# Performance work log

Hardware: AMD Instinct MI355X
Metric: run time of the kernel (lower is better)

## Reference

```python
import jax, jax.numpy as jnp
import numpy as np

B, NQ, NK, D = 4, 4096, 4096, 256


def setup_inputs() -> dict:
    key = jax.random.key(0)
    ks = jax.random.split(key, 14)
    s = 1.0 / np.sqrt(D)
    def lin(k):
        kw, kb = jax.random.split(k)
        return (jax.random.uniform(kw, (D, D), jnp.float32, -s, s),
                jax.random.uniform(kb, (D,), jnp.float32, -s, s))
    Wq, bq = lin(ks[0]); Wk, bk = lin(ks[1]); Wv, bv = lin(ks[2])
    W1, b1 = lin(ks[3]); W2, b2 = lin(ks[4]); W3, b3 = lin(ks[5])
    x = jax.random.normal(ks[6], (B, NK, D), jnp.float32)
    query = jax.random.normal(ks[7], (B, NQ, D), jnp.float32)
    return {"x": x, "query": query,
            "Wq": Wq, "bq": bq, "Wk": Wk, "bk": bk, "Wv": Wv, "bv": bv,
            "W1": W1, "b1": b1, "W2": W2, "b2": b2, "W3": W3, "b3": b3}


def reference(x, query, Wq, bq, Wk, bk, Wv, bv, W1, b1, W2, b2, W3, b3):
    # Linear: y = x @ W.T + b (torch convention)
    q = jnp.einsum('bnd,ed->bne', query, Wq) + bq   # [B,NQ,D]
    k = jnp.einsum('bnd,ed->bne', x, Wk) + bk       # [B,NK,D]
    v = jnp.einsum('bnd,ed->bne', x, Wv) + bv       # [B,NK,D]
    scale = 1.0 / jnp.sqrt(jnp.float32(x.shape[-1]))
    scores = jnp.einsum('bqd,bkd->bqk', q, k) * scale  # [B,NQ,NK]
    attn = jax.nn.softmax(scores, axis=-1)
    out = jnp.einsum('bqk,bkd->bqd', attn, v)          # [B,NQ,D]
    h = jax.nn.relu(jnp.einsum('bqd,ed->bqe', out, W1) + b1)
    h = jax.nn.relu(jnp.einsum('bqd,ed->bqe', h, W2) + b2)
    h = jax.nn.relu(jnp.einsum('bqd,ed->bqe', h, W3) + b3)
    return h, attn
```

## Files before the change

### kernel.cpp

```cpp
#include <hip/hip_runtime.h>

typedef _Float16 h16;
typedef __attribute__((ext_vector_type(4))) _Float16 h16x4;
typedef __attribute__((ext_vector_type(8))) _Float16 h16x8;
typedef __attribute__((ext_vector_type(4))) float f32x4;

#define NQD 4194304L
#define NROWS 16384L
#define NKK 4096L

static __device__ __forceinline__ f32x4 mfma16(h16x8 a, h16x8 b, f32x4 c) {
  return __builtin_amdgcn_mfma_f32_16x16x32_f16(a, b, c, 0, 0, 0);
}

__global__ void cast_weights(const float* __restrict__ w0, const float* __restrict__ w1,
                             const float* __restrict__ w2, const float* __restrict__ w3,
                             const float* __restrict__ w4, const float* __restrict__ w5,
                             h16* __restrict__ dst) {
  int wi = blockIdx.y;
  const float* src = wi == 0 ? w0 : wi == 1 ? w1 : wi == 2 ? w2 : wi == 3 ? w3 : wi == 4 ? w4 : w5;
  int c = blockIdx.x * 256 + threadIdx.x;
  float4 v = ((const float4*)src)[c];
  h16x4 h = {(h16)v.x, (h16)v.y, (h16)v.z, (h16)v.w};
  *(h16x4*)&dst[(long)wi * 65536 + (long)c * 4] = h;
}

__global__ __launch_bounds__(256) void qkv_proj(const float* __restrict__ x,
                                                const float* __restrict__ qry,
                                                const h16* __restrict__ wh,
                                                const float* __restrict__ bq,
                                                const float* __restrict__ bk,
                                                const float* __restrict__ bv,
                                                h16* __restrict__ qh,
                                                h16* __restrict__ kh,
                                                h16* __restrict__ vT) {
  const int z = blockIdx.z;
  const float* A = (z == 0) ? qry : x;
  const h16* W = wh + (long)z * 65536;
  const float* bias = (z == 0) ? bq : (z == 1) ? bk : bv;
  h16* outH = (z == 0) ? qh : (z == 1) ? kh : nullptr;
  h16* outT = (z == 2) ? vT : nullptr;

  __shared__ h16 smem[128 * 72 + 64 * 72];
  h16 (*As)[72] = (h16(*)[72])smem;
  h16 (*Bs)[72] = (h16(*)[72])(smem + 128 * 72);
  const int tid = threadIdx.x;
  const int wave = tid >> 6, lane = tid & 63;
  const int quad = lane >> 4, l16 = lane & 15;
  const long arow0 = (long)blockIdx.x * 128;
  const int bn = blockIdx.y;
  f32x4 acc[2][4] = {};
  for (int k0 = 0; k0 < 256; k0 += 64) {
    #pragma unroll
    for (int it = 0; it < 8; ++it) {
      int c = it * 256 + tid;
      int r = c >> 4, c4 = (c & 15) * 4;
      float4 v = *(const float4*)&A[(arow0 + r) * 256 + k0 + c4];
      h16x4 h = {(h16)v.x, (h16)v.y, (h16)v.z, (h16)v.w};
      *(h16x4*)&As[r][c4] = h;
    }
    #pragma unroll
    for (int it = 0; it < 2; ++it) {
      int c = it * 256 + tid;
      int r = c >> 3, c8 = (c & 7) * 8;
      *(h16x8*)&Bs[r][c8] = *(const h16x8*)&W[(long)(bn * 64 + r) * 256 + k0 + c8];
    }
    __syncthreads();
    #pragma unroll
    for (int ks = 0; ks < 64; ks += 32) {
      h16x8 a[2], b[4];
      #pragma unroll
      for (int mi = 0; mi < 2; ++mi)
        a[mi] = *(const h16x8*)&As[wave * 32 + mi * 16 + l16][ks + quad * 8];
      #pragma unroll
      for (int ni = 0; ni < 4; ++ni)
        b[ni] = *(const h16x8*)&Bs[ni * 16 + l16][ks + quad * 8];
      #pragma unroll
      for (int mi = 0; mi < 2; ++mi)
        #pragma unroll
        for (int ni = 0; ni < 4; ++ni)
          acc[mi][ni] = mfma16(a[mi], b[ni], acc[mi][ni]);
    }
    __syncthreads();
  }
  if (outH) {
    #pragma unroll
    for (int mi = 0; mi < 2; ++mi) {
      #pragma unroll
      for (int ni = 0; ni < 4; ++ni) {
        int n = bn * 64 + ni * 16 + l16;
        float bv_ = bias[n];
        #pragma unroll
        for (int i = 0; i < 4; ++i) {
          long m = arow0 + wave * 32 + mi * 16 + quad * 4 + i;
          outH[m * 256 + n] = (h16)(acc[mi][ni][i] + bv_);
        }
      }
    }
  } else {
    h16* stg = smem;
    #pragma unroll
    for (int mi = 0; mi < 2; ++mi) {
      #pragma unroll
      for (int ni = 0; ni < 4; ++ni) {
        int dl = ni * 16 + l16;
        float bv_ = bias[bn * 64 + dl];
        int mlb = wave * 32 + mi * 16 + quad * 4;
        h16x4 hv = {(h16)(acc[mi][ni][0] + bv_), (h16)(acc[mi][ni][1] + bv_),
                    (h16)(acc[mi][ni][2] + bv_), (h16)(acc[mi][ni][3] + bv_)};
        *(h16x4*)&stg[dl * 136 + mlb] = hv;
      }
    }
    __syncthreads();
    const int bb = (int)(arow0 >> 12);
    const long kb = arow0 & 4095;
    #pragma unroll
    for (int p = 0; p < 4; ++p) {
      int d = p * 16 + (tid >> 4);
      int c = (tid & 15) * 8;
      h16x8 v = *(const h16x8*)&stg[d * 136 + c];
      *(h16x8*)&outT[((long)bb * 256 + bn * 64 + d) * 4096 + kb + c] = v;
    }
  }
}

__global__ __launch_bounds__(256) void gemm256(const h16* __restrict__ A,
                                               const h16* __restrict__ W,
                                               const float* __restrict__ bias,
                                               h16* __restrict__ outH,
                                               float* __restrict__ outF) {
  __shared__ h16 As[128][72];
  __shared__ h16 Bs[64][72];
  const int tid = threadIdx.x;
  const int wave = tid >> 6, lane = tid & 63;
  const int quad = lane >> 4, l16 = lane & 15;
  const long arow0 = (long)blockIdx.x * 128;
  const int bn = blockIdx.y;
  f32x4 acc[2][4] = {};
  for (int k0 = 0; k0 < 256; k0 += 64) {
    #pragma unroll
    for (int it = 0; it < 4; ++it) {
      int c = it * 256 + tid;
      int r = c >> 3, c8 = (c & 7) * 8;
      *(h16x8*)&As[r][c8] = *(const h16x8*)&A[(arow0 + r) * 256 + k0 + c8];
    }
    #pragma unroll
    for (int it = 0; it < 2; ++it) {
      int c = it * 256 + tid;
      int r = c >> 3, c8 = (c & 7) * 8;
      *(h16x8*)&Bs[r][c8] = *(const h16x8*)&W[(long)(bn * 64 + r) * 256 + k0 + c8];
    }
    __syncthreads();
    #pragma unroll
    for (int ks = 0; ks < 64; ks += 32) {
      h16x8 a[2], b[4];
      #pragma unroll
      for (int mi = 0; mi < 2; ++mi)
        a[mi] = *(const h16x8*)&As[wave * 32 + mi * 16 + l16][ks + quad * 8];
      #pragma unroll
      for (int ni = 0; ni < 4; ++ni)
        b[ni] = *(const h16x8*)&Bs[ni * 16 + l16][ks + quad * 8];
      #pragma unroll
      for (int mi = 0; mi < 2; ++mi)
        #pragma unroll
        for (int ni = 0; ni < 4; ++ni)
          acc[mi][ni] = mfma16(a[mi], b[ni], acc[mi][ni]);
    }
    __syncthreads();
  }
  #pragma unroll
  for (int mi = 0; mi < 2; ++mi) {
    #pragma unroll
    for (int ni = 0; ni < 4; ++ni) {
      int n = bn * 64 + ni * 16 + l16;
      float bv = bias[n];
      #pragma unroll
      for (int i = 0; i < 4; ++i) {
        long m = arow0 + wave * 32 + mi * 16 + quad * 4 + i;
        float v = fmaxf(acc[mi][ni][i] + bv, 0.0f);
        if (outH) outH[m * 256 + n] = (h16)v;
        if (outF) outF[m * 256 + n] = v;
      }
    }
  }
}

__global__ __launch_bounds__(256) void gemm_scores(const h16* __restrict__ qh,
                                                   const h16* __restrict__ kh,
                                                   float2* __restrict__ stats,
                                                   h16* __restrict__ Sh,
                                                   float* __restrict__ Sf) {
  __shared__ h16 smem[128 * 72 * 2];
  h16 (*As)[72] = (h16(*)[72])smem;
  h16 (*Bs)[72] = (h16(*)[72])(smem + 128 * 72);
  const int tid = threadIdx.x;
  const int wave = tid >> 6, lane = tid & 63;
  const int quad = lane >> 4, l16 = lane & 15;
  const int bm = blockIdx.x, bn = blockIdx.y, b = blockIdx.z;
  const h16* Aq = qh + (long)b * 4096 * 256 + (long)bm * 128 * 256;
  const h16* Bk = kh + (long)b * 4096 * 256 + (long)bn * 128 * 256;
  f32x4 acc[2][8] = {};
  for (int k0 = 0; k0 < 256; k0 += 64) {
    #pragma unroll
    for (int it = 0; it < 4; ++it) {
      int c = it * 256 + tid;
      int r = c >> 3, c8 = (c & 7) * 8;
      *(h16x8*)&As[r][c8] = *(const h16x8*)&Aq[(long)r * 256 + k0 + c8];
      *(h16x8*)&Bs[r][c8] = *(const h16x8*)&Bk[(long)r * 256 + k0 + c8];
    }
    __syncthreads();
    #pragma unroll
    for (int ks = 0; ks < 64; ks += 32) {
      h16x8 a[2], bb[8];
      #pragma unroll
      for (int mi = 0; mi < 2; ++mi)
        a[mi] = *(const h16x8*)&As[wave * 32 + mi * 16 + l16][ks + quad * 8];
      #pragma unroll
      for (int ni = 0; ni < 8; ++ni)
        bb[ni] = *(const h16x8*)&Bs[ni * 16 + l16][ks + quad * 8];
      #pragma unroll
      for (int mi = 0; mi < 2; ++mi)
        #pragma unroll
        for (int ni = 0; ni < 8; ++ni)
          acc[mi][ni] = mfma16(a[mi], bb[ni], acc[mi][ni]);
    }
    __syncthreads();
  }
  #pragma unroll
  for (int mi = 0; mi < 2; ++mi)
    #pragma unroll
    for (int ni = 0; ni < 8; ++ni)
      #pragma unroll
      for (int i = 0; i < 4; ++i)
        acc[mi][ni][i] *= 0.0625f;
  #pragma unroll
  for (int mi = 0; mi < 2; ++mi) {
    #pragma unroll
    for (int i = 0; i < 4; ++i) {
      float mx = -1e30f;
      #pragma unroll
      for (int ni = 0; ni < 8; ++ni) mx = fmaxf(mx, acc[mi][ni][i]);
      #pragma unroll
      for (int off = 1; off < 16; off <<= 1) mx = fmaxf(mx, __shfl_xor(mx, off));
      float es = 0.0f;
      #pragma unroll
      for (int ni = 0; ni < 8; ++ni) es += __expf(acc[mi][ni][i] - mx);
      #pragma unroll
      for (int off = 1; off < 16; off <<= 1) es += __shfl_xor(es, off);
      if (l16 == 0) {
        long row = (long)b * 4096 + bm * 128 + wave * 32 + mi * 16 + quad * 4 + i;
        stats[row * 32 + bn] = make_float2(mx, es);
      }
    }
  }
  if (Sh) {
    h16* stg = smem;
    #pragma unroll
    for (int mi = 0; mi < 2; ++mi) {
      #pragma unroll
      for (int ni = 0; ni < 8; ++ni) {
        int c = ni * 16 + l16;
        #pragma unroll
        for (int i = 0; i < 4; ++i) {
          int r = wave * 32 + mi * 16 + quad * 4 + i;
          stg[r * 136 + c] = (h16)acc[mi][ni][i];
        }
      }
    }
    __syncthreads();
    const long rowbase = (long)b * 4096 + (long)bm * 128;
    const long colbase = (long)bn * 128;
    #pragma unroll
    for (int p = 0; p < 8; ++p) {
      int r = p * 16 + (tid >> 4);
      int c = (tid & 15) * 8;
      h16x8 v = *(const h16x8*)&stg[r * 136 + c];
      *(h16x8*)&Sh[(rowbase + r) * 4096 + colbase + c] = v;
    }
  } else {
    #pragma unroll
    for (int mi = 0; mi < 2; ++mi) {
      #pragma unroll
      for (int ni = 0; ni < 8; ++ni) {
        long col = (long)bn * 128 + ni * 16 + l16;
        #pragma unroll
        for (int i = 0; i < 4; ++i) {
          long row = (long)b * 4096 + bm * 128 + wave * 32 + mi * 16 + quad * 4 + i;
          Sf[row * 4096 + col] = acc[mi][ni][i];
        }
      }
    }
  }
}

template <typename TS>
__global__ __launch_bounds__(512, 2) void gemm_av(const TS* __restrict__ S,
                                                  const h16* __restrict__ vT,
                                                  const float2* __restrict__ stats,
                                                  float* __restrict__ attn,
                                                  h16* __restrict__ oh) {
  __shared__ h16 As[64][72];
  __shared__ h16 Bs[256][72];
  __shared__ float2 rs[64];
  const int tid = threadIdx.x;
  const int wave = tid >> 6, lane = tid & 63;
  const int quad = lane >> 4, l16 = lane & 15;
  const int mb = blockIdx.x;
  const long row0 = (long)mb * 64;
  const int b = mb >> 6;
  const h16* Vb = vT + (long)b * 256 * 4096;

  {
    int r = tid >> 3, j = tid & 7;
    const float2* sp = stats + (row0 + r) * 32 + j * 4;
    float2 sv4[4];
    float m = -1e30f;
    #pragma unroll
    for (int t = 0; t < 4; ++t) { sv4[t] = sp[t]; m = fmaxf(m, sv4[t].x); }
    m = fmaxf(m, __shfl_xor(m, 1));
    m = fmaxf(m, __shfl_xor(m, 2));
    m = fmaxf(m, __shfl_xor(m, 4));
    float e = 0.0f;
    #pragma unroll
    for (int t = 0; t < 4; ++t) e += sv4[t].y * __expf(sv4[t].x - m);
    e += __shfl_xor(e, 1);
    e += __shfl_xor(e, 2);
    e += __shfl_xor(e, 4);
    if (j == 0) rs[r] = make_float2(m, 1.0f / e);
  }
  __syncthreads();

  const int sr = tid >> 3, sc = (tid & 7) * 8;
  const long srow = row0 + sr;
  const float2 st = rs[sr];
  const TS* Srow = S + srow * 4096;
  float* Arow = attn + srow * 4096;
  const int vd = tid >> 3;

  f32x4 acc[4][2] = {};

  h16x8 sv; float4 sa, sb;
  h16x8 bv0, bv1, bv2, bv3;
  if constexpr (sizeof(TS) == 2) {
    sv = *(const h16x8*)&Srow[sc];
  } else {
    sa = *(const float4*)&Srow[sc];
    sb = *(const float4*)&Srow[sc + 4];
  }
  bv0 = *(const h16x8*)&Vb[(long)(vd)       * 4096 + sc];
  bv1 = *(const h16x8*)&Vb[(long)(vd + 64)  * 4096 + sc];
  bv2 = *(const h16x8*)&Vb[(long)(vd + 128) * 4096 + sc];
  bv3 = *(const h16x8*)&Vb[(long)(vd + 192) * 4096 + sc];

  for (int k0 = 0; k0 < 4096; k0 += 64) {
    float p[8];
    if constexpr (sizeof(TS) == 2) {
      #pragma unroll
      for (int e = 0; e < 8; ++e) p[e] = __expf((float)sv[e] - st.x) * st.y;
    } else {
      p[0] = __expf(sa.x - st.x) * st.y; p[1] = __expf(sa.y - st.x) * st.y;
      p[2] = __expf(sa.z - st.x) * st.y; p[3] = __expf(sa.w - st.x) * st.y;
      p[4] = __expf(sb.x - st.x) * st.y; p[5] = __expf(sb.y - st.x) * st.y;
      p[6] = __expf(sb.z - st.x) * st.y; p[7] = __expf(sb.w - st.x) * st.y;
    }
    f32x4 w0 = {p[0], p[1], p[2], p[3]}, w1 = {p[4], p[5], p[6], p[7]};
    __builtin_nontemporal_store(w0, (f32x4*)&Arow[k0 + sc]);
    __builtin_nontemporal_store(w1, (f32x4*)&Arow[k0 + sc + 4]);
    h16x8 ph = {(h16)p[0], (h16)p[1], (h16)p[2], (h16)p[3],
                (h16)p[4], (h16)p[5], (h16)p[6], (h16)p[7]};
    *(h16x8*)&As[sr][sc] = ph;
    *(h16x8*)&Bs[vd][sc]       = bv0;
    *(h16x8*)&Bs[vd + 64][sc]  = bv1;
    *(h16x8*)&Bs[vd + 128][sc] = bv2;
    *(h16x8*)&Bs[vd + 192][sc] = bv3;
    int kn = k0 + 64;
    if (kn < 4096) {
      if constexpr (sizeof(TS) == 2) {
        sv = *(const h16x8*)&Srow[kn + sc];
      } else {
        sa = *(const float4*)&Srow[kn + sc];
        sb = *(const float4*)&Srow[kn + sc + 4];
      }
      bv0 = *(const h16x8*)&Vb[(long)(vd)       * 4096 + kn + sc];
      bv1 = *(const h16x8*)&Vb[(long)(vd + 64)  * 4096 + kn + sc];
      bv2 = *(const h16x8*)&Vb[(long)(vd + 128) * 4096 + kn + sc];
      bv3 = *(const h16x8*)&Vb[(long)(vd + 192) * 4096 + kn + sc];
    }
    __syncthreads();
    #pragma unroll
    for (int ks = 0; ks < 64; ks += 32) {
      h16x8 a[4], bb[2];
      #pragma unroll
      for (int mi = 0; mi < 4; ++mi)
        a[mi] = *(const h16x8*)&As[mi * 16 + l16][ks + quad * 8];
      #pragma unroll
      for (int ni = 0; ni < 2; ++ni)
        bb[ni] = *(const h16x8*)&Bs[wave * 32 + ni * 16 + l16][ks + quad * 8];
      #pragma unroll
      for (int mi = 0; mi < 4; ++mi)
        #pragma unroll
        for (int ni = 0; ni < 2; ++ni)
          acc[mi][ni] = mfma16(a[mi], bb[ni], acc[mi][ni]);
    }
    __syncthreads();
  }
  h16* stg = &Bs[0][0];
  const int SW = 264;
  #pragma unroll
  for (int mi = 0; mi < 4; ++mi) {
    #pragma unroll
    for (int ni = 0; ni < 2; ++ni) {
      int col = wave * 32 + ni * 16 + l16;
      #pragma unroll
      for (int i = 0; i < 4; ++i) {
        int r = mi * 16 + quad * 4 + i;
        stg[r * SW + col] = (h16)acc[mi][ni][i];
      }
    }
  }
  __syncthreads();
  #pragma unroll
  for (int p = 0; p < 4; ++p) {
    int r = tid >> 3;
    int c = (tid & 7) * 8 + p * 64;
    h16x8 v = *(const h16x8*)&stg[r * SW + c];
    *(h16x8*)&oh[(row0 + r) * 256 + c] = v;
  }
}

extern "C" void kernel_launch(void* const* d_in, const int* in_sizes, int n_in,
                              void* d_out, int out_size, void* d_ws, size_t ws_size,
                              hipStream_t stream) {
  (void)in_sizes; (void)n_in; (void)out_size;
  const float* x   = (const float*)d_in[0];
  const float* qry = (const float*)d_in[1];
  const float* Wq  = (const float*)d_in[2];  const float* bq = (const float*)d_in[3];
  const float* Wk  = (const float*)d_in[4];  const float* bk = (const float*)d_in[5];
  const float* Wv  = (const float*)d_in[6];  const float* bv = (const float*)d_in[7];
  const float* W1  = (const float*)d_in[8];  const float* b1 = (const float*)d_in[9];
  const float* W2  = (const float*)d_in[10]; const float* b2 = (const float*)d_in[11];
  const float* W3  = (const float*)d_in[12]; const float* b3 = (const float*)d_in[13];

  float* outH = (float*)d_out;
  float* attn = outH + NQD;

  char* w = (char*)d_ws;
  h16* qh = (h16*)w;
  h16* kh = qh + NQD;
  h16* vT = kh + NQD;
  h16* oh = vT + NQD;
  h16* h1 = oh + NQD;
  h16* h2 = h1 + NQD;
  h16* wh = h2 + NQD;
  size_t off_rs   = (size_t)(6 * NQD + 6 * 65536) * 2;
  size_t BASE     = off_rs + NROWS * 8;
  size_t statsB   = NROWS * 32 * 8;
  size_t ShB      = NROWS * NKK * 2;

  bool modeA = ws_size >= BASE + statsB + ShB;
  bool modeB = !modeA && ws_size >= BASE + statsB;

  float2* stats = (modeA || modeB) ? (float2*)(w + BASE) : (float2*)h1;
  h16*    Sh    = modeA ? (h16*)(w + BASE + statsB) : nullptr;

  cast_weights<<<dim3(64, 6), 256, 0, stream>>>(Wq, Wk, Wv, W1, W2, W3, wh);
  qkv_proj<<<dim3(128, 4, 3), 256, 0, stream>>>(x, qry, wh, bq, bk, bv, qh, kh, vT);
  gemm_scores<<<dim3(32, 32, 4), 256, 0, stream>>>(qh, kh, stats, Sh, modeA ? nullptr : attn);
  if (modeA)
    gemm_av<h16><<<dim3(256), 512, 0, stream>>>(Sh, vT, stats, attn, oh);
  else
    gemm_av<float><<<dim3(256), 512, 0, stream>>>(attn, vT, stats, attn, oh);
  gemm256<<<dim3(128, 4), 256, 0, stream>>>(oh, wh + 3 * 65536, b1, h1, nullptr);
  gemm256<<<dim3(128, 4), 256, 0, stream>>>(h1, wh + 4 * 65536, b2, h2, nullptr);
  gemm256<<<dim3(128, 4), 256, 0, stream>>>(h2, wh + 5 * 65536, b3, nullptr, outH);
}
```

Measured before the change: 550.3 us.

## Split attention-times-V kernel into smaller 32-row, half-D tiles with direct V loads

Adds gemm_av2, which tiles the P·V product as 32 query rows by 128 output columns. That gives a 512x2 grid of 256-thread blocks instead of 256 blocks of 512 threads, to raise occupancy and spread work across more CUs. V fragments are loaded straight from global memory into registers instead of being staged through shared memory. Only the ny==0 blocks write the fp32 attention probabilities, using nontemporal stores. The cost is that each S row is read and exponentiated twice, once per column half, and the V loads are no longer shared across waves.

```diff
diff --git a/kernel.cpp b/kernel.cpp
--- a/kernel.cpp
+++ b/kernel.cpp
@@ -290,6 +290,103 @@
         }
       }
     }
+  }
+}
+
+__global__ __launch_bounds__(256, 4) void gemm_av2(const h16* __restrict__ S,
+                                                   const h16* __restrict__ vT,
+                                                   const float2* __restrict__ stats,
+                                                   float* __restrict__ attn,
+                                                   h16* __restrict__ oh) {
+  __shared__ h16 As[32][72];
+  __shared__ h16 stg[32][136];
+  __shared__ float2 rs[32];
+  const int tid = threadIdx.x;
+  const int wave = tid >> 6, lane = tid & 63;
+  const int quad = lane >> 4, l16 = lane & 15;
+  const int mb = blockIdx.x, ny = blockIdx.y;
+  const long row0 = (long)mb * 32;
+  const int b = mb >> 7;
+  const h16* Vb = vT + (long)b * 256 * 4096 + ((long)ny * 128) * 4096;
+
+  {
+    int r = tid >> 3, j = tid & 7;
+    const float2* sp = stats + (row0 + r) * 32 + j * 4;
+    float2 sv4[4];
+    float m = -1e30f;
+    #pragma unroll
+    for (int t = 0; t < 4; ++t) { sv4[t] = sp[t]; m = fmaxf(m, sv4[t].x); }
+    m = fmaxf(m, __shfl_xor(m, 1));
+    m = fmaxf(m, __shfl_xor(m, 2));
+    m = fmaxf(m, __shfl_xor(m, 4));
+    float e = 0.0f;
+    #pragma unroll
+    for (int t = 0; t < 4; ++t) e += sv4[t].y * __expf(sv4[t].x - m);
+    e += __shfl_xor(e, 1);
+    e += __shfl_xor(e, 2);
+    e += __shfl_xor(e, 4);
+    if (j == 0) rs[r] = make_float2(m, 1.0f / e);
+  }
+  __syncthreads();
+
+  const int sr = tid >> 3, sc = (tid & 7) * 8;
+  const long srow = row0 + sr;
+  const float2 st = rs[sr];
+  const h16* Srow = S + srow * 4096;
+  float* Arow = attn + srow * 4096;
+
+  f32x4 acc[2][2] = {};
+  h16x8 sv = *(const h16x8*)&Srow[sc];
+
+  for (int k0 = 0; k0 < 4096; k0 += 64) {
+    float p[8];
+    #pragma unroll
+    for (int e = 0; e < 8; ++e) p[e] = __expf((float)sv[e] - st.x) * st.y;
+    if (ny == 0) {
+      f32x4 w0 = {p[0], p[1], p[2], p[3]}, w1 = {p[4], p[5], p[6], p[7]};
+      __builtin_nontemporal_store(w0, (f32x4*)&Arow[k0 + sc]);
+      __builtin_nontemporal_store(w1, (f32x4*)&Arow[k0 + sc + 4]);
+    }
+    h16x8 ph = {(h16)p[0], (h16)p[1], (h16)p[2], (h16)p[3],
+                (h16)p[4], (h16)p[5], (h16)p[6], (h16)p[7]};
+    *(h16x8*)&As[sr][sc] = ph;
+    h16x8 bb[2][2];
+    #pragma unroll
+    for (int ks2 = 0; ks2 < 2; ++ks2)
+      #pragma unroll
+      for (int ni = 0; ni < 2; ++ni)
+        bb[ks2][ni] = *(const h16x8*)&Vb[(long)(wave * 32 + ni * 16 + l16) * 4096 + k0 + ks2 * 32 + quad * 8];
+    int kn = k0 + 64;
+    if (kn < 4096) sv = *(const h16x8*)&Srow[kn + sc];
+    __syncthreads();
+    #pragma unroll
+    for (int ks2 = 0; ks2 < 2; ++ks2) {
+      h16x8 a0 = *(const h16x8*)&As[l16][ks2 * 32 + quad * 8];
+      h16x8 a1 = *(const h16x8*)&As[16 + l16][ks2 * 32 + quad * 8];
+      acc[0][0] = mfma16(a0, bb[ks2][0], acc[0][0]);
+      acc[0][1] = mfma16(a0, bb[ks2][1], acc[0][1]);
+      acc[1][0] = mfma16(a1, bb[ks2][0], acc[1][0]);
+      acc[1][1] = mfma16(a1, bb[ks2][1], acc[1][1]);
+    }
+    __syncthreads();
+  }
+  #pragma unroll
+  for (int mi = 0; mi < 2; ++mi) {
+    #pragma unroll
+    for (int ni = 0; ni < 2; ++ni) {
+      int col = wave * 32 + ni * 16 + l16;
+      #pragma unroll
+      for (int i = 0; i < 4; ++i)
+        stg[mi * 16 + quad * 4 + i][col] = (h16)acc[mi][ni][i];
+    }
+  }
+  __syncthreads();
+  #pragma unroll
+  for (int p = 0; p < 2; ++p) {
+    int r = tid >> 3;
+    int c = (tid & 7) * 8 + p * 64;
+    h16x8 v = *(const h16x8*)&stg[r][c];
+    *(h16x8*)&oh[(row0 + r) * 256 + ny * 128 + c] = v;
   }
 }
 
@@ -389,18 +486,18 @@
     __syncthreads();
     #pragma unroll
     for (int ks = 0; ks < 64; ks += 32) {
-      h16x8 a[4], bb[2];
+      h16x8 a[4], bbv[2];
       #pragma unroll
       for (int mi = 0; mi < 4; ++mi)
         a[mi] = *(const h16x8*)&As[mi * 16 + l16][ks + quad * 8];
       #pragma unroll
       for (int ni = 0; ni < 2; ++ni)
-        bb[ni] = *(const h16x8*)&Bs[wave * 32 + ni * 16 + l16][ks + quad * 8];
+        bbv[ni] = *(const h16x8*)&Bs[wave * 32 + ni * 16 + l16][ks + quad * 8];
       #pragma unroll
       for (int mi = 0; mi < 4; ++mi)
         #pragma unroll
         for (int ni = 0; ni < 2; ++ni)
-          acc[mi][ni] = mfma16(a[mi], bb[ni], acc[mi][ni]);
+          acc[mi][ni] = mfma16(a[mi], bbv[ni], acc[mi][ni]);
     }
     __syncthreads();
   }
@@ -467,7 +564,7 @@
   qkv_proj<<<dim3(128, 4, 3), 256, 0, stream>>>(x, qry, wh, bq, bk, bv, qh, kh, vT);
   gemm_scores<<<dim3(32, 32, 4), 256, 0, stream>>>(qh, kh, stats, Sh, modeA ? nullptr : attn);
   if (modeA)
-    gemm_av<h16><<<dim3(256), 512, 0, stream>>>(Sh, vT, stats, attn, oh);
+    gemm_av2<<<dim3(512, 2), 256, 0, stream>>>(Sh, vT, stats, attn, oh);
   else
     gemm_av<float><<<dim3(256), 512, 0, stream>>>(attn, vT, stats, attn, oh);
   gemm256<<<dim3(128, 4), 256, 0, stream>>>(oh, wh + 3 * 65536, b1, h1, nullptr);
```

After: 613.8 us. 11.5% more time.
